# Optimization experiments

Measured on AMD Instinct MI355X. Metric: run time of the kernel, lower is better.

The kernel has to match this reference:

```python
import jax, jax.numpy as jnp
import numpy as np
from jax import lax

B, T, ENC = 32, 300, 1024
H, A, C, K = 512, 256, 10, 100
V, E, AO = 10000, 512, 512
TD = 80
BOS = 1
SCALING = 2.0


def setup_inputs() -> dict:
    key = jax.random.key(0)
    ks = jax.random.split(key, 20)
    def mat(k, shape, fan_in):
        return jax.random.normal(k, shape, dtype=jnp.float32) / np.sqrt(fan_in)
    enc_pad = jax.random.normal(ks[0], (B, T, ENC), dtype=jnp.float32)
    enc_len = jax.random.randint(ks[1], (B,), T // 2, T + 1, dtype=jnp.int32)
    return {
        "enc_pad": enc_pad,
        "enc_len": enc_len,
        "embedding": mat(ks[2], (V, E), E),
        "W_ih": mat(ks[3], (4 * H, E + AO), E + AO),
        "b_ih": jnp.zeros((4 * H,), jnp.float32),
        "W_hh": mat(ks[4], (4 * H, H), H),
        "b_hh": jnp.zeros((4 * H,), jnp.float32),
        "W_enc": mat(ks[5], (A, ENC), ENC),
        "b_enc": jnp.zeros((A,), jnp.float32),
        "W_dec": mat(ks[6], (A, H), H),
        "W_att": mat(ks[7], (A, C), C),
        "conv_k": mat(ks[8], (C, 1, 2 * K + 1), 2 * K + 1),  # Conv2d(1,C,(1,2K+1)) collapsed to 1D
        "W_g": mat(ks[9], (1, A), A),
        "W_o": mat(ks[10], (AO, ENC), ENC),
        "b_o": jnp.zeros((AO,), jnp.float32),
        "W_out": mat(ks[11], (V, H + AO), H + AO),
        "b_out": jnp.zeros((V,), jnp.float32),
    }


def reference(enc_pad, enc_len, embedding, W_ih, b_ih, W_hh, b_hh,
              W_enc, b_enc, W_dec, W_att, conv_k, W_g, W_o, b_o, W_out, b_out):
    # pre-compute encoder projection once (AttLoc.pre_compute_enc_h)
    pre_enc = jnp.einsum('btd,ad->bta', enc_pad, W_enc) + b_enc  # [B,T,A]
    lens = enc_len.astype(jnp.float32)
    # initial att weights: uniform 1/l over valid frames, 0 on padding
    mask = (jnp.arange(T)[None, :] < enc_len[:, None]).astype(jnp.float32)
    w0 = mask / lens[:, None]
    dec_z0 = jnp.zeros((B, H), jnp.float32)
    dec_c0 = jnp.zeros((B, H), jnp.float32)
    c0 = jnp.zeros((B, AO), jnp.float32)
    prev0 = jnp.full((B,), BOS, dtype=jnp.int32)

    def step(carry, _):
        dec_z, dec_c, c, w, prev = carry
        emb = embedding[prev]                                    # [B,E]
        x = jnp.concatenate([emb, c], axis=-1)                   # [B,E+AO]
        gates = x @ W_ih.T + b_ih + dec_z @ W_hh.T + b_hh        # [B,4H]
        i, f, g, o = jnp.split(gates, 4, axis=-1)
        dec_c = jax.nn.sigmoid(f) * dec_c + jax.nn.sigmoid(i) * jnp.tanh(g)
        dec_z = jax.nn.sigmoid(o) * jnp.tanh(dec_c)
        # location-aware attention
        conv = lax.conv_general_dilated(
            w[:, None, :], conv_k, (1,), [(K, K)],
            dimension_numbers=('NCH', 'OIH', 'NCH'))             # [B,C,T]
        att_conv = jnp.einsum('bct,ac->bta', conv, W_att)        # [B,T,A]
        dec_t = (dec_z @ W_dec.T)[:, None, :]                    # [B,1,A]
        e = jnp.einsum('bta,a->bt', jnp.tanh(pre_enc + dec_t + att_conv), W_g[0])
        w = jax.nn.softmax(SCALING * e, axis=1)                  # [B,T]
        cvec = jnp.einsum('bt,btd->bd', w, enc_pad) @ W_o.T + b_o  # [B,AO]
        logit = jnp.concatenate([dec_z, cvec], axis=-1) @ W_out.T + b_out  # [B,V]
        pred = jnp.argmax(logit, axis=-1).astype(jnp.int32)
        return (dec_z, dec_c, cvec, w, pred), (logit, w, pred)

    _, (logits, ws, preds) = lax.scan(step, (dec_z0, dec_c0, c0, w0, prev0),
                                      None, length=TD)
    logits = jnp.swapaxes(logits, 0, 1)        # [B,TD,V]
    ws = jnp.swapaxes(ws, 0, 1)                # [B,TD,T]
    preds = jnp.swapaxes(preds, 0, 1)          # [B,TD]
    log_probs = jax.nn.log_softmax(logits, axis=2)
    ys_log_probs = jnp.take_along_axis(log_probs, preds[..., None], axis=2)[..., 0]
    return logits, ys_log_probs, preds, ws
```

## Files before the change

### kernel.cpp

```cpp
#include <hip/hip_runtime.h>
#include <math.h>

#define NB   32
#define NT   300
#define NE   1024
#define NH   512
#define NA   256
#define NC   10
#define NKW  201
#define NV   10000
#define NEMB 512
#define NAO  512
#define NTD  80
#define SCL  2.0f

__device__ __forceinline__ float sigf(float x){ return 1.f/(1.f+expf(-x)); }

__global__ __launch_bounds__(256) void k_init(const int* __restrict__ enc_len,
    float* __restrict__ zbuf, float* __restrict__ cA, float* __restrict__ cvp,
    float* __restrict__ wbuf, int* __restrict__ prev)
{
    int i = blockIdx.x*256 + threadIdx.x;
    if (i < NB*NH)   { zbuf[i]=0.f; cA[i]=0.f; }
    if (i < 4*NB*NAO)  cvp[i]=0.f;
    if (i < NB*NT)   { int b=i/NT, t=i%NT; int len=enc_len[b];
                       wbuf[i] = (t<len)? 1.f/(float)len : 0.f; }
    if (i < NB)        prev[i]=1;
}

__global__ __launch_bounds__(256) void k_gemm_pre(const float* __restrict__ Ag,
    const float* __restrict__ Wg, const float* __restrict__ bias,
    float* __restrict__ Cg, int N)
{
    __shared__ float As[32][68];
    __shared__ float Bs[32][68];
    const int tid = threadIdx.x;
    const int m0 = blockIdx.y*64, n0 = blockIdx.x*64;
    const int r  = tid>>2, kg = (tid&3)*8;
    const int ty = tid>>4, tx = tid&15;
    float acc[4][4] = {};
    for (int k0 = 0; k0 < 1024; k0 += 32) {
        const float4 a0 = *(const float4*)(Ag + (size_t)(m0+r)*1024 + k0+kg);
        const float4 a1 = *(const float4*)(Ag + (size_t)(m0+r)*1024 + k0+kg+4);
        const float4 b0 = *(const float4*)(Wg + (size_t)(n0+r)*1024 + k0+kg);
        const float4 b1 = *(const float4*)(Wg + (size_t)(n0+r)*1024 + k0+kg+4);
        __syncthreads();
        As[kg+0][r]=a0.x; As[kg+1][r]=a0.y; As[kg+2][r]=a0.z; As[kg+3][r]=a0.w;
        As[kg+4][r]=a1.x; As[kg+5][r]=a1.y; As[kg+6][r]=a1.z; As[kg+7][r]=a1.w;
        Bs[kg+0][r]=b0.x; Bs[kg+1][r]=b0.y; Bs[kg+2][r]=b0.z; Bs[kg+3][r]=b0.w;
        Bs[kg+4][r]=b1.x; Bs[kg+5][r]=b1.y; Bs[kg+6][r]=b1.z; Bs[kg+7][r]=b1.w;
        __syncthreads();
        #pragma unroll
        for (int kk=0; kk<32; ++kk) {
            const float4 av = *(const float4*)&As[kk][ty*4];
            const float4 bv = *(const float4*)&Bs[kk][tx*4];
            const float a[4]={av.x,av.y,av.z,av.w};
            const float bb[4]={bv.x,bv.y,bv.z,bv.w};
            #pragma unroll
            for (int i=0;i<4;++i)
                #pragma unroll
                for (int j=0;j<4;++j) acc[i][j] += a[i]*bb[j];
        }
    }
    #pragma unroll
    for (int i=0;i<4;++i){
        const int m = m0 + ty*4 + i;
        #pragma unroll
        for (int j=0;j<4;++j)
            Cg[(size_t)m*N + n0 + tx*4 + j] = acc[i][j] + bias[n0+tx*4+j];
    }
}

__global__ __launch_bounds__(256) void k_gates(const float* __restrict__ emb,
    const int* __restrict__ prev, const float* __restrict__ cp,
    const float* __restrict__ zbuf, const float* __restrict__ W_ih,
    const float* __restrict__ W_hh, float* __restrict__ gp)
{
    __shared__ float xt[32][68];
    const int tid = threadIdx.x;
    const int kp  = blockIdx.y;
    const int lane = tid&63, wv = tid>>6;
    const int bs = lane&15, nsl = lane>>4;
    const int n0 = blockIdx.x*32 + wv*8 + nsl*2;
    const int sb = tid>>3, sk = (tid&7)*8;
    const int pvs = prev[sb];
    const float* wih0 = W_ih + (size_t)n0*1024;
    const float* whh0 = W_hh + (size_t)n0*512;
    float a00=0.f,a01=0.f,a10=0.f,a11=0.f;
    for (int tile=0; tile<6; ++tile) {
        const int k0 = kp*384 + tile*64;
        const int gk = k0 + sk;
        float4 v0, v1;
        if (gk < 512) {
            const float4* p = (const float4*)(emb + (size_t)pvs*NEMB + gk);
            v0 = p[0]; v1 = p[1];
        } else if (gk < 1024) {
            const int off = gk-512;
            const float4* p0 = (const float4*)(cp + sb*NAO + off);
            const float4* p1 = (const float4*)(cp + NB*NAO + sb*NAO + off);
            const float4* p2 = (const float4*)(cp + 2*NB*NAO + sb*NAO + off);
            const float4* p3 = (const float4*)(cp + 3*NB*NAO + sb*NAO + off);
            const float4 a0=p0[0], a1=p1[0], a2=p2[0], a3=p3[0];
            const float4 b0=p0[1], b1=p1[1], b2=p2[1], b3=p3[1];
            v0 = make_float4(a0.x+a1.x+a2.x+a3.x, a0.y+a1.y+a2.y+a3.y,
                             a0.z+a1.z+a2.z+a3.z, a0.w+a1.w+a2.w+a3.w);
            v1 = make_float4(b0.x+b1.x+b2.x+b3.x, b0.y+b1.y+b2.y+b3.y,
                             b0.z+b1.z+b2.z+b3.z, b0.w+b1.w+b2.w+b3.w);
        } else {
            const float4* p = (const float4*)(zbuf + sb*NH + (gk-1024));
            v0 = p[0]; v1 = p[1];
        }
        __syncthreads();
        *(float4*)&xt[sb][sk]   = v0;
        *(float4*)&xt[sb][sk+4] = v1;
        __syncthreads();
        const float* w0 = (k0 < 1024) ? wih0 + k0        : whh0 + (k0-1024);
        const float* w1 = (k0 < 1024) ? wih0 + 1024 + k0 : whh0 + 512 + (k0-1024);
        #pragma unroll
        for (int c=0;c<16;++c){
            const float4 xa = *(const float4*)&xt[bs][c*4];
            const float4 xb = *(const float4*)&xt[bs+16][c*4];
            const float4 wa = *(const float4*)(w0 + c*4);
            const float4 wb = *(const float4*)(w1 + c*4);
            a00 += xa.x*wa.x+xa.y*wa.y+xa.z*wa.z+xa.w*wa.w;
            a01 += xa.x*wb.x+xa.y*wb.y+xa.z*wb.z+xa.w*wb.w;
            a10 += xb.x*wa.x+xb.y*wa.y+xb.z*wa.z+xb.w*wa.w;
            a11 += xb.x*wb.x+xb.y*wb.y+xb.z*wb.z+xb.w*wb.w;
        }
    }
    float* g = gp + (size_t)(kp*NB)*2048;
    g[(size_t)bs*2048 + n0]        = a00;
    g[(size_t)bs*2048 + n0+1]      = a01;
    g[(size_t)(bs+16)*2048 + n0]   = a10;
    g[(size_t)(bs+16)*2048 + n0+1] = a11;
}

__global__ __launch_bounds__(256) void k_attn(
    const float* __restrict__ gp, const float* __restrict__ b_ih,
    const float* __restrict__ b_hh, const float* __restrict__ cin,
    float* __restrict__ cout, float* __restrict__ zbuf,
    const float* __restrict__ W_dec, const float* __restrict__ pre_enc,
    const float* __restrict__ wbuf, const float* __restrict__ ck,
    const float* __restrict__ W_att, const float* __restrict__ W_g,
    float* __restrict__ ebuf)
{
    __shared__ float zs[NH];
    __shared__ float w_h[260];
    __shared__ float ck_s[NC*NKW];
    __shared__ float wt_s[NA*NC];
    __shared__ float dt_s[NA];
    __shared__ float wg_s[NA];
    __shared__ float cv_s[60*NC];
    __shared__ float ep_s[60][4];
    const int tid = threadIdx.x;
    const int b = blockIdx.y, t0 = blockIdx.x*60;
    for (int h = tid; h < NH; h += 256) {
        float g[4];
        #pragma unroll
        for (int r=0;r<4;++r){
            float s = b_ih[r*512+h] + b_hh[r*512+h];
            #pragma unroll
            for (int kp=0;kp<4;++kp) s += gp[(size_t)(kp*NB+b)*2048 + r*512 + h];
            g[r]=s;
        }
        const float c = sigf(g[1])*cin[b*NH+h] + sigf(g[0])*tanhf(g[2]);
        const float z = sigf(g[3])*tanhf(c);
        zs[h] = z;
        if (blockIdx.x==0){ cout[b*NH+h]=c; zbuf[b*NH+h]=z; }
    }
    for (int i=tid;i<260;i+=256){ const int gt=t0-100+i;
        w_h[i] = (gt>=0 && gt<NT)? wbuf[b*NT+gt] : 0.f; }
    for (int i=tid;i<NC*NKW;i+=256) ck_s[i]=ck[i];
    for (int i=tid;i<NA*NC;i+=256)  wt_s[i]=W_att[i];
    wg_s[tid] = W_g[tid];
    __syncthreads();
    {
        const int grp = tid>>3, l = tid&7;
        float4 zr[16];
        #pragma unroll
        for (int q=0;q<16;++q) zr[q] = *(const float4*)&zs[l*4 + q*32];
        #pragma unroll
        for (int j=0;j<8;++j){
            const int a = grp*8 + j;
            const float* w = W_dec + (size_t)a*NH;
            float sv = 0.f;
            #pragma unroll
            for (int q=0;q<16;++q){
                const float4 wv4 = *(const float4*)(w + l*4 + q*32);
                sv += zr[q].x*wv4.x + zr[q].y*wv4.y + zr[q].z*wv4.z + zr[q].w*wv4.w;
            }
            sv += __shfl_down(sv, 4, 8);
            sv += __shfl_down(sv, 2, 8);
            sv += __shfl_down(sv, 1, 8);
            if (l==0) dt_s[a] = sv;
        }
    }
    __syncthreads();
    for (int i=tid;i<60*NC;i+=256){
        const int tl=i/NC, ch=i%NC;
        float s=0.f;
        const float* wp  = &w_h[tl];
        const float* ckp = &ck_s[ch*NKW];
        for (int k=0;k<NKW;++k) s += wp[k]*ckp[k];
        cv_s[i]=s;
    }
    __syncthreads();
    const int tq = tid&3, tl = tid>>2;
    if (tl < 60) {
        float cv[NC];
        #pragma unroll
        for (int ch=0;ch<NC;++ch) cv[ch]=cv_s[tl*NC+ch];
        const float* pe = pre_enc + (size_t)(b*NT + t0 + tl)*NA;
        float part=0.f;
        for (int i=0;i<64;++i){
            const int aa = tq + 4*i;
            float attc = 0.f;
            #pragma unroll
            for (int ch=0;ch<NC;++ch) attc += cv[ch]*wt_s[aa*NC+ch];
            part += tanhf(pe[aa] + dt_s[aa] + attc) * wg_s[aa];
        }
        ep_s[tl][tq] = part;
    }
    __syncthreads();
    if (tid < 60)
        ebuf[b*NT + t0 + tid] = ep_s[tid][0]+ep_s[tid][1]+ep_s[tid][2]+ep_s[tid][3];
}

__global__ __launch_bounds__(256) void k_ctxsm(const float* __restrict__ ebuf,
    const float* __restrict__ enc_o, float* __restrict__ cvp,
    float* __restrict__ wbuf, float* __restrict__ out_ws, int step)
{
    __shared__ float es[NT], wsm[NT], red[256];
    const int tid=threadIdx.x;
    const int b = blockIdx.x>>3, q = blockIdx.x&7;
    const int th = q>>1, oc = q&1;
    for (int t=tid;t<NT;t+=256) es[t]=ebuf[b*NT+t];
    __syncthreads();
    float m=-3.4e38f;
    for (int t=tid;t<NT;t+=256) m=fmaxf(m,es[t]);
    red[tid]=m; __syncthreads();
    for (int r=128;r>0;r>>=1){ if(tid<r) red[tid]=fmaxf(red[tid],red[tid+r]); __syncthreads(); }
    m=red[0]; __syncthreads();
    float ss=0.f;
    for (int t=tid;t<NT;t+=256) ss+=expf(SCL*(es[t]-m));
    red[tid]=ss; __syncthreads();
    for (int r=128;r>0;r>>=1){ if(tid<r) red[tid]+=red[tid+r]; __syncthreads(); }
    const float inv = 1.f/red[0];
    for (int t=tid;t<NT;t+=256){
        const float w = expf(SCL*(es[t]-m))*inv;
        wsm[t]=w;
        if (q==0){ wbuf[b*NT+t]=w; out_ws[((size_t)b*NTD+step)*NT+t]=w; }
    }
    __syncthreads();
    const int o = oc*256 + tid;
    const float* ep = enc_o + ((size_t)b*NT + th*75)*NAO + o;
    float acc=0.f;
    #pragma unroll
    for (int t=0;t<75;++t) acc += wsm[th*75+t]*ep[(size_t)t*NAO];
    cvp[(size_t)(th*NB+b)*NAO + o] = acc;
}

__global__ __launch_bounds__(256) void k_logits(const float* __restrict__ zbuf,
    const float* __restrict__ cp, const float* __restrict__ W_out,
    float* __restrict__ lp)
{
    __shared__ float xt[32][68];
    const int tid=threadIdx.x, kp=blockIdx.y;
    const int lane=tid&63, wv=tid>>6, bs=lane&15, nsl=lane>>4;
    const int n0 = blockIdx.x*32 + wv*8 + nsl*2;
    const int rn0 = (n0   < NV)? n0   : NV-1;
    const int rn1 = (n0+1 < NV)? n0+1 : NV-1;
    const float* w0 = W_out + (size_t)rn0*1024;
    const float* w1 = W_out + (size_t)rn1*1024;
    const int sb = tid>>3, sk = (tid&7)*8;
    float a00=0.f,a01=0.f,a10=0.f,a11=0.f;
    for (int tile=0; tile<4; ++tile) {
        const int k0 = kp*256 + tile*64;
        const int gk = k0 + sk;
        float4 v0, v1;
        if (gk < 512) {
            const float4* p = (const float4*)(zbuf + sb*NH + gk);
            v0 = p[0]; v1 = p[1];
        } else {
            const int off = gk-512;
            const float4* p0 = (const float4*)(cp + sb*NAO + off);
            const float4* p1 = (const float4*)(cp + NB*NAO + sb*NAO + off);
            const float4* p2 = (const float4*)(cp + 2*NB*NAO + sb*NAO + off);
            const float4* p3 = (const float4*)(cp + 3*NB*NAO + sb*NAO + off);
            const float4 a0=p0[0], a1=p1[0], a2=p2[0], a3=p3[0];
            const float4 b0=p0[1], b1=p1[1], b2=p2[1], b3=p3[1];
            v0 = make_float4(a0.x+a1.x+a2.x+a3.x, a0.y+a1.y+a2.y+a3.y,
                             a0.z+a1.z+a2.z+a3.z, a0.w+a1.w+a2.w+a3.w);
            v1 = make_float4(b0.x+b1.x+b2.x+b3.x, b0.y+b1.y+b2.y+b3.y,
                             b0.z+b1.z+b2.z+b3.z, b0.w+b1.w+b2.w+b3.w);
        }
        __syncthreads();
        *(float4*)&xt[sb][sk]   = v0;
        *(float4*)&xt[sb][sk+4] = v1;
        __syncthreads();
        #pragma unroll
        for (int c=0;c<16;++c){
            const float4 xa = *(const float4*)&xt[bs][c*4];
            const float4 xb = *(const float4*)&xt[bs+16][c*4];
            const float4 wa = *(const float4*)(w0 + k0 + c*4);
            const float4 wb = *(const float4*)(w1 + k0 + c*4);
            a00 += xa.x*wa.x+xa.y*wa.y+xa.z*wa.z+xa.w*wa.w;
            a01 += xa.x*wb.x+xa.y*wb.y+xa.z*wb.z+xa.w*wb.w;
            a10 += xb.x*wa.x+xb.y*wa.y+xb.z*wa.z+xb.w*wa.w;
            a11 += xb.x*wb.x+xb.y*wb.y+xb.z*wb.z+xb.w*wb.w;
        }
    }
    if (n0 < NV){
        lp[(size_t)(kp*NB+bs)*NV + n0]    = a00;
        lp[(size_t)(kp*NB+bs+16)*NV + n0] = a10;
    }
    if (n0+1 < NV){
        lp[(size_t)(kp*NB+bs)*NV + n0+1]    = a01;
        lp[(size_t)(kp*NB+bs+16)*NV + n0+1] = a11;
    }
}

__global__ __launch_bounds__(256) void k_fin(const float* __restrict__ lp,
    const float* __restrict__ b_out, int step, float* __restrict__ out_logits,
    int* __restrict__ prev, float* __restrict__ out_preds, float* __restrict__ out_ylp)
{
    __shared__ float rv[256];
    __shared__ int   ri[256];
    const int b=blockIdx.x, tid=threadIdx.x;
    const float* p0 = lp + (size_t)b*NV;
    const float* p1 = lp + (size_t)(NB+b)*NV;
    const float* p2 = lp + (size_t)(2*NB+b)*NV;
    const float* p3 = lp + (size_t)(3*NB+b)*NV;
    float* dst = out_logits + ((size_t)b*NTD + step)*NV;
    float m=-3.4e38f; int mi=NV;
    for (int v=tid; v<NV; v+=256){
        const float l = p0[v]+p1[v]+p2[v]+p3[v]+b_out[v];
        dst[v]=l;
        if (l>m){ m=l; mi=v; }
    }
    rv[tid]=m; ri[tid]=mi; __syncthreads();
    for (int s=128;s>0;s>>=1){
        if (tid<s){
            if (rv[tid+s]>rv[tid] || (rv[tid+s]==rv[tid] && ri[tid+s]<ri[tid])){
                rv[tid]=rv[tid+s]; ri[tid]=ri[tid+s];
            }
        }
        __syncthreads();
    }
    m=rv[0]; mi=ri[0]; __syncthreads();
    float ss=0.f;
    for (int v=tid; v<NV; v+=256) ss += expf(dst[v]-m);
    rv[tid]=ss; __syncthreads();
    for (int s=128;s>0;s>>=1){ if(tid<s) rv[tid]+=rv[tid+s]; __syncthreads(); }
    if (tid==0){
        prev[b]=mi;
        out_preds[b*NTD+step]=(float)mi;
        out_ylp[b*NTD+step]=-logf(rv[0]);
    }
}

extern "C" void kernel_launch(void* const* d_in, const int* in_sizes, int n_in,
                              void* d_out, int out_size, void* d_ws, size_t ws_size,
                              hipStream_t stream)
{
    const float* enc_pad   = (const float*)d_in[0];
    const int*   enc_len   = (const int*)d_in[1];
    const float* embedding = (const float*)d_in[2];
    const float* W_ih      = (const float*)d_in[3];
    const float* b_ih      = (const float*)d_in[4];
    const float* W_hh      = (const float*)d_in[5];
    const float* b_hh      = (const float*)d_in[6];
    const float* W_enc     = (const float*)d_in[7];
    const float* b_enc     = (const float*)d_in[8];
    const float* W_dec     = (const float*)d_in[9];
    const float* W_att     = (const float*)d_in[10];
    const float* conv_k    = (const float*)d_in[11];
    const float* W_g       = (const float*)d_in[12];
    const float* W_o       = (const float*)d_in[13];
    const float* b_o       = (const float*)d_in[14];
    const float* W_out     = (const float*)d_in[15];
    const float* b_out     = (const float*)d_in[16];

    float* out_logits = (float*)d_out;
    float* out_ylp    = out_logits + (size_t)NB*NTD*NV;
    float* out_preds  = out_ylp + NB*NTD;
    float* out_ws     = out_preds + NB*NTD;

    float* f = (float*)d_ws;
    float* pre_enc = f;
    float* enc_o   = pre_enc + (size_t)NB*NT*NA;
    float* zbuf    = enc_o + (size_t)NB*NT*NAO;
    float* cA      = zbuf + NB*NH;
    float* cB      = cA + NB*NH;
    float* gp      = cB + NB*NH;
    float* cvp     = gp + 4*NB*2048;
    float* ebuf    = cvp + 4*NB*NAO;
    float* wbuf    = ebuf + NB*NT;
    float* lp      = wbuf + NB*NT;
    int*   prev    = (int*)(lp + (size_t)4*NB*NV);

    k_init<<<256, 256, 0, stream>>>(enc_len, zbuf, cA, cvp, wbuf, prev);
    k_gemm_pre<<<dim3(NA/64,  NB*NT/64), 256, 0, stream>>>(enc_pad, W_enc, b_enc, pre_enc, NA);
    k_gemm_pre<<<dim3(NAO/64, NB*NT/64), 256, 0, stream>>>(enc_pad, W_o,   b_o,   enc_o,   NAO);

    for (int s = 0; s < NTD; ++s) {
        float* cin  = (s & 1) ? cB : cA;
        float* cout = (s & 1) ? cA : cB;
        k_gates <<<dim3(64,4),  256, 0, stream>>>(embedding, prev, cvp, zbuf, W_ih, W_hh, gp);
        k_attn  <<<dim3(5,32),  256, 0, stream>>>(gp, b_ih, b_hh, cin, cout, zbuf,
                                                  W_dec, pre_enc, wbuf, conv_k, W_att, W_g, ebuf);
        k_ctxsm <<<256,         256, 0, stream>>>(ebuf, enc_o, cvp, wbuf, out_ws, s);
        k_logits<<<dim3(313,4), 256, 0, stream>>>(zbuf, cvp, W_out, lp);
        k_fin   <<<32,          256, 0, stream>>>(lp, b_out, s, out_logits, prev,
                                                  out_preds, out_ylp);
    }
}
```

Measured before the change: 10.54 ms.

## Fuse softmax/context into attention and argmax into logits via atomic grid barriers

Merges the context/softmax kernel into the attention kernel using a per-batch atomic spin barrier across the 5 time-chunk blocks, and merges the final logit reduction/argmax into the logits kernel, where the last 32 blocks to arrive wait on a counter and then do the per-batch reduction. This cuts the per-step launch count from five to three. Context partials now come from 5 chunks instead of 4, and the attention weights are double-buffered. The spin barriers rely on all participating blocks being co-resident, which risks deadlock, and the elected blocks stall while they wait.

Result: slower. 19.96 ms (+89.4%).

```diff
diff --git a/kernel.cpp b/kernel.cpp
--- a/kernel.cpp
+++ b/kernel.cpp
@@ -13,19 +13,24 @@
 #define NAO  512
 #define NTD  80
 #define SCL  2.0f
+#define NLOGB 1252
+#define NELECT 32
 
 __device__ __forceinline__ float sigf(float x){ return 1.f/(1.f+expf(-x)); }
 
 __global__ __launch_bounds__(256) void k_init(const int* __restrict__ enc_len,
     float* __restrict__ zbuf, float* __restrict__ cA, float* __restrict__ cvp,
-    float* __restrict__ wbuf, int* __restrict__ prev)
+    float* __restrict__ wbuf, int* __restrict__ prev, int* __restrict__ abar,
+    int* __restrict__ lbar)
 {
     int i = blockIdx.x*256 + threadIdx.x;
-    if (i < NB*NH)   { zbuf[i]=0.f; cA[i]=0.f; }
-    if (i < 4*NB*NAO)  cvp[i]=0.f;
-    if (i < NB*NT)   { int b=i/NT, t=i%NT; int len=enc_len[b];
-                       wbuf[i] = (t<len)? 1.f/(float)len : 0.f; }
-    if (i < NB)        prev[i]=1;
+    if (i < NB*NH)    { zbuf[i]=0.f; cA[i]=0.f; }
+    if (i < 5*NB*NAO)   cvp[i]=0.f;
+    if (i < NB*NT)    { int b=i/NT, t=i%NT; int len=enc_len[b];
+                        wbuf[i] = (t<len)? 1.f/(float)len : 0.f; }
+    if (i < NB)         prev[i]=1;
+    if (i < NTD*NB)     abar[i]=0;
+    if (i < NTD)        lbar[i]=0;
 }
 
 __global__ __launch_bounds__(256) void k_gemm_pre(const float* __restrict__ Ag,
@@ -96,16 +101,16 @@
             v0 = p[0]; v1 = p[1];
         } else if (gk < 1024) {
             const int off = gk-512;
-            const float4* p0 = (const float4*)(cp + sb*NAO + off);
-            const float4* p1 = (const float4*)(cp + NB*NAO + sb*NAO + off);
-            const float4* p2 = (const float4*)(cp + 2*NB*NAO + sb*NAO + off);
-            const float4* p3 = (const float4*)(cp + 3*NB*NAO + sb*NAO + off);
-            const float4 a0=p0[0], a1=p1[0], a2=p2[0], a3=p3[0];
-            const float4 b0=p0[1], b1=p1[1], b2=p2[1], b3=p3[1];
-            v0 = make_float4(a0.x+a1.x+a2.x+a3.x, a0.y+a1.y+a2.y+a3.y,
-                             a0.z+a1.z+a2.z+a3.z, a0.w+a1.w+a2.w+a3.w);
-            v1 = make_float4(b0.x+b1.x+b2.x+b3.x, b0.y+b1.y+b2.y+b3.y,
-                             b0.z+b1.z+b2.z+b3.z, b0.w+b1.w+b2.w+b3.w);
+            float4 s0 = make_float4(0.f,0.f,0.f,0.f);
+            float4 s1 = make_float4(0.f,0.f,0.f,0.f);
+            #pragma unroll
+            for (int j=0;j<5;++j){
+                const float4* p = (const float4*)(cp + (size_t)j*NB*NAO + sb*NAO + off);
+                const float4 u0=p[0], u1=p[1];
+                s0.x+=u0.x; s0.y+=u0.y; s0.z+=u0.z; s0.w+=u0.w;
+                s1.x+=u1.x; s1.y+=u1.y; s1.z+=u1.z; s1.w+=u1.w;
+            }
+            v0 = s0; v1 = s1;
         } else {
             const float4* p = (const float4*)(zbuf + sb*NH + (gk-1024));
             v0 = p[0]; v1 = p[1];
@@ -140,9 +145,11 @@
     const float* __restrict__ b_hh, const float* __restrict__ cin,
     float* __restrict__ cout, float* __restrict__ zbuf,
     const float* __restrict__ W_dec, const float* __restrict__ pre_enc,
-    const float* __restrict__ wbuf, const float* __restrict__ ck,
+    const float* __restrict__ win, const float* __restrict__ ck,
     const float* __restrict__ W_att, const float* __restrict__ W_g,
-    float* __restrict__ ebuf)
+    float* __restrict__ ebuf, const float* __restrict__ enc_o,
+    float* __restrict__ cvp, float* __restrict__ wout,
+    float* __restrict__ out_ws, int* __restrict__ abar, int step)
 {
     __shared__ float zs[NH];
     __shared__ float w_h[260];
@@ -152,8 +159,11 @@
     __shared__ float wg_s[NA];
     __shared__ float cv_s[60*NC];
     __shared__ float ep_s[60][4];
+    __shared__ float es[NT];
+    __shared__ float wsm[NT];
+    __shared__ float red[256];
     const int tid = threadIdx.x;
-    const int b = blockIdx.y, t0 = blockIdx.x*60;
+    const int b = blockIdx.y, x = blockIdx.x, t0 = x*60;
     for (int h = tid; h < NH; h += 256) {
         float g[4];
         #pragma unroll
@@ -166,10 +176,10 @@
         const float c = sigf(g[1])*cin[b*NH+h] + sigf(g[0])*tanhf(g[2]);
         const float z = sigf(g[3])*tanhf(c);
         zs[h] = z;
-        if (blockIdx.x==0){ cout[b*NH+h]=c; zbuf[b*NH+h]=z; }
+        if (x==0){ cout[b*NH+h]=c; zbuf[b*NH+h]=z; }
     }
     for (int i=tid;i<260;i+=256){ const int gt=t0-100+i;
-        w_h[i] = (gt>=0 && gt<NT)? wbuf[b*NT+gt] : 0.f; }
+        w_h[i] = (gt>=0 && gt<NT)? win[b*NT+gt] : 0.f; }
     for (int i=tid;i<NC*NKW;i+=256) ck_s[i]=ck[i];
     for (int i=tid;i<NA*NC;i+=256)  wt_s[i]=W_att[i];
     wg_s[tid] = W_g[tid];
@@ -224,16 +234,16 @@
     __syncthreads();
     if (tid < 60)
         ebuf[b*NT + t0 + tid] = ep_s[tid][0]+ep_s[tid][1]+ep_s[tid][2]+ep_s[tid][3];
-}
-
-__global__ __launch_bounds__(256) void k_ctxsm(const float* __restrict__ ebuf,
-    const float* __restrict__ enc_o, float* __restrict__ cvp,
-    float* __restrict__ wbuf, float* __restrict__ out_ws, int step)
-{
-    __shared__ float es[NT], wsm[NT], red[256];
-    const int tid=threadIdx.x;
-    const int b = blockIdx.x>>3, q = blockIdx.x&7;
-    const int th = q>>1, oc = q&1;
+    __syncthreads();
+    if (tid==0){
+        __threadfence();
+        __hip_atomic_fetch_add(&abar[step*NB+b], 1, __ATOMIC_ACQ_REL,
+                               __HIP_MEMORY_SCOPE_AGENT);
+        while (__hip_atomic_load(&abar[step*NB+b], __ATOMIC_ACQUIRE,
+                                 __HIP_MEMORY_SCOPE_AGENT) < 5) {}
+    }
+    __syncthreads();
+    __threadfence();
     for (int t=tid;t<NT;t+=256) es[t]=ebuf[b*NT+t];
     __syncthreads();
     float m=-3.4e38f;
@@ -249,22 +259,32 @@
     for (int t=tid;t<NT;t+=256){
         const float w = expf(SCL*(es[t]-m))*inv;
         wsm[t]=w;
-        if (q==0){ wbuf[b*NT+t]=w; out_ws[((size_t)b*NTD+step)*NT+t]=w; }
-    }
-    __syncthreads();
-    const int o = oc*256 + tid;
-    const float* ep = enc_o + ((size_t)b*NT + th*75)*NAO + o;
-    float acc=0.f;
-    #pragma unroll
-    for (int t=0;t<75;++t) acc += wsm[th*75+t]*ep[(size_t)t*NAO];
-    cvp[(size_t)(th*NB+b)*NAO + o] = acc;
+        if (x==0){ wout[b*NT+t]=w; out_ws[((size_t)b*NTD+step)*NT+t]=w; }
+    }
+    __syncthreads();
+    const float* ep2 = enc_o + ((size_t)b*NT + t0)*NAO;
+    float acc0=0.f, acc1=0.f;
+    #pragma unroll 4
+    for (int t=0;t<60;++t){
+        const float w = wsm[t0+t];
+        acc0 += w*ep2[(size_t)t*NAO + tid];
+        acc1 += w*ep2[(size_t)t*NAO + tid + 256];
+    }
+    cvp[(size_t)(x*NB+b)*NAO + tid]       = acc0;
+    cvp[(size_t)(x*NB+b)*NAO + tid + 256] = acc1;
 }
 
 __global__ __launch_bounds__(256) void k_logits(const float* __restrict__ zbuf,
     const float* __restrict__ cp, const float* __restrict__ W_out,
-    float* __restrict__ lp)
+    float* __restrict__ lp, const float* __restrict__ b_out, int step,
+    float* __restrict__ out_logits, int* __restrict__ prev,
+    float* __restrict__ out_preds, float* __restrict__ out_ylp,
+    int* __restrict__ lbar)
 {
     __shared__ float xt[32][68];
+    __shared__ float rv[256];
+    __shared__ int   ri[256];
+    __shared__ int   relect;
     const int tid=threadIdx.x, kp=blockIdx.y;
     const int lane=tid&63, wv=tid>>6, bs=lane&15, nsl=lane>>4;
     const int n0 = blockIdx.x*32 + wv*8 + nsl*2;
@@ -283,16 +303,16 @@
             v0 = p[0]; v1 = p[1];
         } else {
             const int off = gk-512;
-            const float4* p0 = (const float4*)(cp + sb*NAO + off);
-            const float4* p1 = (const float4*)(cp + NB*NAO + sb*NAO + off);
-            const float4* p2 = (const float4*)(cp + 2*NB*NAO + sb*NAO + off);
-            const float4* p3 = (const float4*)(cp + 3*NB*NAO + sb*NAO + off);
-            const float4 a0=p0[0], a1=p1[0], a2=p2[0], a3=p3[0];
-            const float4 b0=p0[1], b1=p1[1], b2=p2[1], b3=p3[1];
-            v0 = make_float4(a0.x+a1.x+a2.x+a3.x, a0.y+a1.y+a2.y+a3.y,
-                             a0.z+a1.z+a2.z+a3.z, a0.w+a1.w+a2.w+a3.w);
-            v1 = make_float4(b0.x+b1.x+b2.x+b3.x, b0.y+b1.y+b2.y+b3.y,
-                             b0.z+b1.z+b2.z+b3.z, b0.w+b1.w+b2.w+b3.w);
+            float4 s0 = make_float4(0.f,0.f,0.f,0.f);
+            float4 s1 = make_float4(0.f,0.f,0.f,0.f);
+            #pragma unroll
+            for (int j=0;j<5;++j){
+                const float4* p = (const float4*)(cp + (size_t)j*NB*NAO + sb*NAO + off);
+                const float4 u0=p[0], u1=p[1];
+                s0.x+=u0.x; s0.y+=u0.y; s0.z+=u0.z; s0.w+=u0.w;
+                s1.x+=u1.x; s1.y+=u1.y; s1.z+=u1.z; s1.w+=u1.w;
+            }
+            v0 = s0; v1 = s1;
         }
         __syncthreads();
         *(float4*)&xt[sb][sk]   = v0;
@@ -318,44 +338,51 @@
         lp[(size_t)(kp*NB+bs)*NV + n0+1]    = a01;
         lp[(size_t)(kp*NB+bs+16)*NV + n0+1] = a11;
     }
-}
-
-__global__ __launch_bounds__(256) void k_fin(const float* __restrict__ lp,
-    const float* __restrict__ b_out, int step, float* __restrict__ out_logits,
-    int* __restrict__ prev, float* __restrict__ out_preds, float* __restrict__ out_ylp)
-{
-    __shared__ float rv[256];
-    __shared__ int   ri[256];
-    const int b=blockIdx.x, tid=threadIdx.x;
-    const float* p0 = lp + (size_t)b*NV;
-    const float* p1 = lp + (size_t)(NB+b)*NV;
-    const float* p2 = lp + (size_t)(2*NB+b)*NV;
-    const float* p3 = lp + (size_t)(3*NB+b)*NV;
-    float* dst = out_logits + ((size_t)b*NTD + step)*NV;
-    float m=-3.4e38f; int mi=NV;
-    for (int v=tid; v<NV; v+=256){
-        const float l = p0[v]+p1[v]+p2[v]+p3[v]+b_out[v];
-        dst[v]=l;
-        if (l>m){ m=l; mi=v; }
-    }
-    rv[tid]=m; ri[tid]=mi; __syncthreads();
-    for (int s=128;s>0;s>>=1){
-        if (tid<s){
-            if (rv[tid+s]>rv[tid] || (rv[tid+s]==rv[tid] && ri[tid+s]<ri[tid])){
-                rv[tid]=rv[tid+s]; ri[tid]=ri[tid+s];
+    __syncthreads();
+    if (tid==0){
+        __threadfence();
+        int r = __hip_atomic_fetch_add(&lbar[step], 1, __ATOMIC_ACQ_REL,
+                                       __HIP_MEMORY_SCOPE_AGENT);
+        relect = r;
+        if (r >= NLOGB-NELECT){
+            while (__hip_atomic_load(&lbar[step], __ATOMIC_ACQUIRE,
+                                     __HIP_MEMORY_SCOPE_AGENT) < NLOGB) {}
+        }
+    }
+    __syncthreads();
+    if (relect >= NLOGB-NELECT){
+        __threadfence();
+        const int b = relect - (NLOGB-NELECT);
+        const float* p0 = lp + (size_t)b*NV;
+        const float* p1 = lp + (size_t)(NB+b)*NV;
+        const float* p2 = lp + (size_t)(2*NB+b)*NV;
+        const float* p3 = lp + (size_t)(3*NB+b)*NV;
+        float* dst = out_logits + ((size_t)b*NTD + step)*NV;
+        float m=-3.4e38f; int mi=NV;
+        for (int v=tid; v<NV; v+=256){
+            const float l = p0[v]+p1[v]+p2[v]+p3[v]+b_out[v];
+            dst[v]=l;
+            if (l>m){ m=l; mi=v; }
+        }
+        rv[tid]=m; ri[tid]=mi; __syncthreads();
+        for (int s=128;s>0;s>>=1){
+            if (tid<s){
+                if (rv[tid+s]>rv[tid] || (rv[tid+s]==rv[tid] && ri[tid+s]<ri[tid])){
+                    rv[tid]=rv[tid+s]; ri[tid]=ri[tid+s];
+                }
             }
-        }
-        __syncthreads();
-    }
-    m=rv[0]; mi=ri[0]; __syncthreads();
-    float ss=0.f;
-    for (int v=tid; v<NV; v+=256) ss += expf(dst[v]-m);
-    rv[tid]=ss; __syncthreads();
-    for (int s=128;s>0;s>>=1){ if(tid<s) rv[tid]+=rv[tid+s]; __syncthreads(); }
-    if (tid==0){
-        prev[b]=mi;
-        out_preds[b*NTD+step]=(float)mi;
-        out_ylp[b*NTD+step]=-logf(rv[0]);
+            __syncthreads();
+        }
+        m=rv[0]; mi=ri[0]; __syncthreads();
+        float ss=0.f;
+        for (int v=tid; v<NV; v+=256) ss += expf(dst[v]-m);
+        rv[tid]=ss; __syncthreads();
+        for (int s=128;s>0;s>>=1){ if(tid<s) rv[tid]+=rv[tid+s]; __syncthreads(); }
+        if (tid==0){
+            prev[b]=mi;
+            out_preds[b*NTD+step]=(float)mi;
+            out_ylp[b*NTD+step]=-logf(rv[0]);
+        }
     }
 }
 
@@ -394,24 +421,28 @@
     float* cB      = cA + NB*NH;
     float* gp      = cB + NB*NH;
     float* cvp     = gp + 4*NB*2048;
-    float* ebuf    = cvp + 4*NB*NAO;
-    float* wbuf    = ebuf + NB*NT;
-    float* lp      = wbuf + NB*NT;
+    float* ebuf    = cvp + 5*NB*NAO;
+    float* wA      = ebuf + NB*NT;
+    float* wB      = wA + NB*NT;
+    float* lp      = wB + NB*NT;
     int*   prev    = (int*)(lp + (size_t)4*NB*NV);
-
-    k_init<<<256, 256, 0, stream>>>(enc_len, zbuf, cA, cvp, wbuf, prev);
+    int*   abar    = prev + NB;
+    int*   lbar    = abar + NTD*NB;
+
+    k_init<<<512, 256, 0, stream>>>(enc_len, zbuf, cA, cvp, wA, prev, abar, lbar);
     k_gemm_pre<<<dim3(NA/64,  NB*NT/64), 256, 0, stream>>>(enc_pad, W_enc, b_enc, pre_enc, NA);
     k_gemm_pre<<<dim3(NAO/64, NB*NT/64), 256, 0, stream>>>(enc_pad, W_o,   b_o,   enc_o,   NAO);
 
     for (int s = 0; s < NTD; ++s) {
         float* cin  = (s & 1) ? cB : cA;
         float* cout = (s & 1) ? cA : cB;
+        float* win  = (s & 1) ? wB : wA;
+        float* wout = (s & 1) ? wA : wB;
         k_gates <<<dim3(64,4),  256, 0, stream>>>(embedding, prev, cvp, zbuf, W_ih, W_hh, gp);
         k_attn  <<<dim3(5,32),  256, 0, stream>>>(gp, b_ih, b_hh, cin, cout, zbuf,
-                                                  W_dec, pre_enc, wbuf, conv_k, W_att, W_g, ebuf);
-        k_ctxsm <<<256,         256, 0, stream>>>(ebuf, enc_o, cvp, wbuf, out_ws, s);
-        k_logits<<<dim3(313,4), 256, 0, stream>>>(zbuf, cvp, W_out, lp);
-        k_fin   <<<32,          256, 0, stream>>>(lp, b_out, s, out_logits, prev,
-                                                  out_preds, out_ylp);
-    }
-}
+                                                  W_dec, pre_enc, win, conv_k, W_att, W_g,
+                                                  ebuf, enc_o, cvp, wout, out_ws, abar, s);
+        k_logits<<<dim3(313,4), 256, 0, stream>>>(zbuf, cvp, W_out, lp, b_out, s,
+                                                  out_logits, prev, out_preds, out_ylp, lbar);
+    }
+}
```
